# Optimization experiments

Hardware: AMD Instinct MI355X
Metric: run time of the kernel (lower is better)

The kernel has to match this reference:

```python
import jax, jax.numpy as jnp
import numpy as np

S, B, D = 2048, 2, 4096
H, KVH, HD = 32, 8, 128          # n_heads_q, n_kv_heads, head_dim
NREP = H // KVH                  # GQA repeat factor
ROPE_BASE = 10000.0


def _rope(x, cos, sin):
    # x: [B, S, h, HD]; cos/sin: [S, HD//2]
    xr = x.reshape(x.shape[:-1] + (-1, 2))
    x0, x1 = xr[..., 0], xr[..., 1]
    c = cos[None, :, None, :]
    s = sin[None, :, None, :]
    out = jnp.stack([x0 * c - x1 * s, x0 * s + x1 * c], axis=-1)
    return out.reshape(x.shape)


def setup_inputs() -> dict:
    key = jax.random.key(0)
    k0, k1, k2, k3, k4 = jax.random.split(key, 5)
    x = jax.random.normal(k0, (S, B, D), jnp.float32)
    inv_freq = 1.0 / (ROPE_BASE ** (np.arange(0, HD, 2, dtype=np.float64) / HD))  # [HD//2]
    t = np.arange(S, dtype=np.float64)[:, None] * inv_freq[None, :]               # [S, HD//2]
    freqs_cos = jnp.asarray(np.cos(t), jnp.float32)
    freqs_sin = jnp.asarray(np.sin(t), jnp.float32)
    scale = 0.02
    wq = jax.random.normal(k1, (H * HD, D), jnp.float32) * scale
    wk = jax.random.normal(k2, (KVH * HD, D), jnp.float32) * scale
    wv = jax.random.normal(k3, (KVH * HD, D), jnp.float32) * scale
    wo = jax.random.normal(k4, (D, H * HD), jnp.float32) * scale
    return {"x": x, "start_pos": 0, "freqs_cos": freqs_cos, "freqs_sin": freqs_sin,
            "wq": wq, "wk": wk, "wv": wv, "wo": wo}


def reference(x, start_pos, freqs_cos, freqs_sin, wq, wk, wv, wo):
    seq_len, batch, _ = x.shape
    # QKV projections (torch Linear: y = x @ W^T), then [S,B,*] -> [B,S,h,HD]
    q = (x @ wq.T).transpose(1, 0, 2).reshape(batch, seq_len, H, HD)
    k = (x @ wk.T).transpose(1, 0, 2).reshape(batch, seq_len, KVH, HD)
    v = (x @ wv.T).transpose(1, 0, 2).reshape(batch, seq_len, KVH, HD)
    # RoPE on q and k
    q = _rope(q, freqs_cos, freqs_sin)
    k = _rope(k, freqs_cos, freqs_sin)
    # repeat_kv (GQA)
    k = jnp.repeat(k, NREP, axis=2)
    v = jnp.repeat(v, NREP, axis=2)
    # [B, H, S, HD]
    q = q.transpose(0, 2, 1, 3)
    k = k.transpose(0, 2, 1, 3)
    v = v.transpose(0, 2, 1, 3)
    # causal scaled dot-product attention (SDPA is_causal=True equivalent)
    scores = jnp.einsum('bhqd,bhkd->bhqk', q, k) / np.float32(np.sqrt(HD))
    causal = jnp.tril(jnp.ones((seq_len, seq_len), dtype=bool))
    scores = jnp.where(causal[None, None], scores, jnp.float32(-jnp.inf))
    probs = jax.nn.softmax(scores.astype(jnp.float32), axis=-1).astype(q.dtype)
    out = jnp.einsum('bhqk,bhkd->bhqd', probs, v)
    # [B,H,S,HD] -> [B,S,H*HD] -> [S,B,H*HD]
    out = out.transpose(0, 2, 1, 3).reshape(batch, seq_len, H * HD).transpose(1, 0, 2)
    return out @ wo.T
```

## Files before the change

### kernel.cpp

```cpp
#include <hip/hip_runtime.h>

typedef __attribute__((ext_vector_type(8))) short s16x8;
typedef __attribute__((ext_vector_type(8))) __bf16 bf16x8;
typedef __attribute__((ext_vector_type(4))) float f32x4;

#define S_LEN 2048
#define KDIM  4096
#define CSOFT 0.12751743f

__device__ __forceinline__ unsigned short f2bf(float f) {
  unsigned u = __builtin_bit_cast(unsigned, f);
  u += 0x7fffu + ((u >> 16) & 1u);
  return (unsigned short)(u >> 16);
}

__device__ __forceinline__ f32x4 mfma_bf16(s16x8 a, s16x8 b, f32x4 c) {
  return __builtin_amdgcn_mfma_f32_16x16x32_bf16(
      __builtin_bit_cast(bf16x8, a), __builtin_bit_cast(bf16x8, b), c, 0, 0, 0);
}

__device__ __forceinline__ void gload_lds16(const unsigned short* g, void* l) {
  __builtin_amdgcn_global_load_lds(
      (const __attribute__((address_space(1))) void*)g,
      (__attribute__((address_space(3))) void*)l, 16, 0, 0);
}

__global__ void cvt_bf16(const float* __restrict__ in,
                         unsigned short* __restrict__ out, int n8) {
  int i = blockIdx.x * 256 + threadIdx.x;
  if (i >= n8) return;
  const float* p = in + (size_t)i * 8;
  f32x4 a = *(const f32x4*)(p);
  f32x4 b = *(const f32x4*)(p + 4);
  s16x8 v;
  v[0] = (short)f2bf(a[0]); v[1] = (short)f2bf(a[1]);
  v[2] = (short)f2bf(a[2]); v[3] = (short)f2bf(a[3]);
  v[4] = (short)f2bf(b[0]); v[5] = (short)f2bf(b[1]);
  v[6] = (short)f2bf(b[2]); v[7] = (short)f2bf(b[3]);
  *(s16x8*)(out + (size_t)i * 8) = v;
}

template <int EPI>
__global__ __launch_bounds__(512, 1)
void gemm256(const unsigned short* __restrict__ A,
             const unsigned short* __restrict__ B,
             void* __restrict__ Out,
             const float* __restrict__ cosT,
             const float* __restrict__ sinT) {
  const int K = KDIM;
  __shared__ __align__(16) unsigned short As[2 * 2 * 8192];
  __shared__ __align__(16) unsigned short Bs[2 * 2 * 8192];

  const int tid = threadIdx.x;
  const int lane = tid & 63, wid = tid >> 6;
  const int l15 = lane & 15, l4 = lane >> 4;
  const int wr = wid >> 2, wc = wid & 3;

  int bid = blockIdx.x;
  int wg = (bid & 7) * 32 + (bid >> 3);
  const int rt = wg >> 4, ct = wg & 15;
  const int row0 = rt * 256, col0 = ct * 256;

  const int ch0 = tid, ch1 = 512 + tid;
  const int sr0 = ch0 >> 3, u0 = (ch0 & 7) ^ (sr0 & 7);
  const int sr1 = ch1 >> 3, u1 = (ch1 & 7) ^ (sr1 & 7);
  const unsigned short* A0p = A + (size_t)(row0 + sr0) * K + u0 * 8;
  const unsigned short* A1p = A + (size_t)(row0 + sr1) * K + u1 * 8;
  const unsigned short* B0p = B + (size_t)(col0 + sr0) * K + u0 * 8;
  const unsigned short* B1p = B + (size_t)(col0 + sr1) * K + u1 * 8;

  const int rdo0 = l15 * 128 + ((l4 ^ (l15 & 7)) << 4);
  const int rdo1 = l15 * 128 + (((4 | l4) ^ (l15 & 7)) << 4);

  f32x4 acc[8][4];
#pragma unroll
  for (int m = 0; m < 8; m++)
#pragma unroll
    for (int n = 0; n < 4; n++) acc[m][n] = f32x4{0.f, 0.f, 0.f, 0.f};

  auto stageA = [&](int buf, int h, int kt) {
    char* d = (char*)As + buf * 32768 + h * 16384 + wid * 1024;
    size_t so = (size_t)h * 128 * K + kt;
    gload_lds16(A0p + so, d);
    gload_lds16(A1p + so, d + 8192);
  };
  auto stageB = [&](int buf, int h, int kt) {
    char* d = (char*)Bs + buf * 32768 + h * 16384 + wid * 1024;
    size_t so = (size_t)h * 128 * K + kt;
    gload_lds16(B0p + so, d);
    gload_lds16(B1p + so, d + 8192);
  };
  auto bar = [&]() {
    __builtin_amdgcn_s_barrier();
    __builtin_amdgcn_sched_barrier(0);
  };
  auto quad = [&](const s16x8* ak0, const s16x8* ak1,
                  const s16x8* bk0, const s16x8* bk1, int mb, int nb) {
    __builtin_amdgcn_s_setprio(1);
#pragma unroll
    for (int mi = 0; mi < 4; mi++)
#pragma unroll
      for (int ni = 0; ni < 2; ni++) {
        acc[mb + mi][nb + ni] =
            mfma_bf16(ak0[mi], bk0[ni], acc[mb + mi][nb + ni]);
        acc[mb + mi][nb + ni] =
            mfma_bf16(ak1[mi], bk1[ni], acc[mb + mi][nb + ni]);
      }
    __builtin_amdgcn_s_setprio(0);
  };

  auto tile4 = [&](int buf, auto st1, auto st2, auto st3, auto st4,
                   int vmEnd) {
    const char* Ab = (const char*)As + buf * 32768 + wr * 16384;
    const char* Bb = (const char*)Bs + buf * 32768 + (wc >> 1) * 16384 +
                     (wc & 1) * 8192;
    s16x8 a0k0[4], a0k1[4], a1k0[4], a1k1[4];
    s16x8 b0k0[2], b0k1[2], b1k0[2], b1k1[2];

#pragma unroll
    for (int mi = 0; mi < 4; mi++) {
      a0k0[mi] = *(const s16x8*)(Ab + mi * 2048 + rdo0);
      a0k1[mi] = *(const s16x8*)(Ab + mi * 2048 + rdo1);
    }
#pragma unroll
    for (int ni = 0; ni < 2; ni++) {
      b0k0[ni] = *(const s16x8*)(Bb + ni * 2048 + rdo0);
      b0k1[ni] = *(const s16x8*)(Bb + ni * 2048 + rdo1);
    }
    st1();
    bar();
    quad(a0k0, a0k1, b0k0, b0k1, 0, 0);
    bar();

#pragma unroll
    for (int mi = 0; mi < 4; mi++) {
      a1k0[mi] = *(const s16x8*)(Ab + 8192 + mi * 2048 + rdo0);
      a1k1[mi] = *(const s16x8*)(Ab + 8192 + mi * 2048 + rdo1);
    }
#pragma unroll
    for (int ni = 0; ni < 2; ni++) {
      b1k0[ni] = *(const s16x8*)(Bb + 4096 + ni * 2048 + rdo0);
      b1k1[ni] = *(const s16x8*)(Bb + 4096 + ni * 2048 + rdo1);
    }
    st2();
    bar();
    quad(a1k0, a1k1, b0k0, b0k1, 4, 0);
    bar();

    st3();
    bar();
    quad(a0k0, a0k1, b1k0, b1k1, 0, 2);
    bar();

    st4();
    bar();
    quad(a1k0, a1k1, b1k0, b1k1, 4, 2);
    if (vmEnd == 4) {
      asm volatile("s_waitcnt vmcnt(4)" ::: "memory");
    } else if (vmEnd == 0) {
      asm volatile("s_waitcnt vmcnt(0)" ::: "memory");
    }
    bar();
  };
  auto nop = [&]() {};

  stageA(0, 0, 0);
  stageA(0, 1, 0);
  stageB(0, 0, 0);
  stageB(0, 1, 0);
  stageA(1, 0, 64);
  stageA(1, 1, 64);
  asm volatile("s_waitcnt vmcnt(4)" ::: "memory");
  bar();

  for (int j = 0; j < 31; j++) {
    const int k1 = (2 * j + 1) * 64, k2 = (2 * j + 2) * 64,
              k3 = (2 * j + 3) * 64;
    tile4(0, [&] { stageB(1, 0, k1); }, [&] { stageB(1, 1, k1); },
          [&] { stageA(0, 0, k2); }, [&] { stageA(0, 1, k2); }, 4);
    tile4(1, [&] { stageB(0, 0, k2); }, [&] { stageB(0, 1, k2); },
          [&] { stageA(1, 0, k3); }, [&] { stageA(1, 1, k3); }, 4);
  }
  {
    const int k1 = 63 * 64;
    tile4(0, [&] { stageB(1, 0, k1); }, [&] { stageB(1, 1, k1); }, nop, nop,
          0);
    tile4(1, nop, nop, nop, nop, -1);
  }

#pragma unroll
  for (int m = 0; m < 8; m++) {
#pragma unroll
    for (int n = 0; n < 4; n++) {
      f32x4 v = acc[m][n];
      int rowb = row0 + wr * 128 + m * 16 + l4 * 4;
      int col = col0 + wc * 64 + n * 16 + l15;
      if (EPI == 3) {
        float* o = (float*)Out;
#pragma unroll
        for (int r = 0; r < 4; r++) o[(size_t)(rowb + r) * 4096 + col] = v[r];
      } else {
        float vp[4];
#pragma unroll
        for (int r = 0; r < 4; r++) vp[r] = __shfl_xor(v[r], 1, 64);
        bool odd = lane & 1;
        int fi = (col & 127) >> 1;
#pragma unroll
        for (int r = 0; r < 4; r++) {
          int nn = rowb + r, s = nn >> 1;
          float c = cosT[s * 64 + fi], sn = sinT[s * 64 + fi];
          v[r] = odd ? (vp[r] * sn + v[r] * c) : (v[r] * c - vp[r] * sn);
        }
        unsigned short* o = (unsigned short*)Out;
        int hh = col >> 7, hd = col & 127;
#pragma unroll
        for (int r = 0; r < 4; r++) {
          int nn = rowb + r, s = nn >> 1, b = nn & 1;
          o[((size_t)(b * 32 + hh) * 2048 + s) * 128 + hd] = f2bf(v[r]);
        }
      }
    }
  }
}

template <int EPI, int N, bool B_FP32>
__global__ __launch_bounds__(256, 2)
void gemm_bt(const unsigned short* __restrict__ A,
             const float* __restrict__ Bw32,
             const unsigned short* __restrict__ Bw16,
             void* __restrict__ Out,
             const float* __restrict__ cosT,
             const float* __restrict__ sinT) {
  const int K = KDIM;
  const int tid = threadIdx.x;
  const int lane = tid & 63, wid = tid >> 6;
  const int l15 = lane & 15, l4 = lane >> 4;
  const int nct = N / 128;
  const int ct = blockIdx.x % nct, rt = blockIdx.x / nct;
  const int row0 = rt * 128, col0 = ct * 128;
  const int wr = wid >> 1, wc = wid & 1;

  __shared__ __align__(16) unsigned short As[128 * 32];
  __shared__ __align__(16) unsigned short Bs[128 * 32];

  f32x4 acc[4][4];
#pragma unroll
  for (int i = 0; i < 4; i++)
#pragma unroll
    for (int j = 0; j < 4; j++) acc[i][j] = f32x4{0.f, 0.f, 0.f, 0.f};

  for (int kt = 0; kt < K; kt += 32) {
#pragma unroll
    for (int i = 0; i < 2; i++) {
      int j = wid * 2 + i;
      int ch = j * 64 + lane;
      int r = ch >> 2, c = ch & 3;
      int sc = c ^ ((r >> 1) & 3);
      gload_lds16(A + (size_t)(row0 + r) * K + kt + sc * 8, (char*)As + j * 1024);
    }
    if (B_FP32) {
#pragma unroll
      for (int j = 0; j < 2; j++) {
        int ch = tid + 256 * j;
        int r = ch >> 2, c = ch & 3;
        const float* src = Bw32 + (size_t)(col0 + r) * K + kt + c * 8;
        f32x4 f0 = *(const f32x4*)(src);
        f32x4 f1 = *(const f32x4*)(src + 4);
        s16x8 v;
        v[0] = (short)f2bf(f0[0]); v[1] = (short)f2bf(f0[1]);
        v[2] = (short)f2bf(f0[2]); v[3] = (short)f2bf(f0[3]);
        v[4] = (short)f2bf(f1[0]); v[5] = (short)f2bf(f1[1]);
        v[6] = (short)f2bf(f1[2]); v[7] = (short)f2bf(f1[3]);
        int sw = c ^ ((r >> 1) & 3);
        *(s16x8*)((char*)Bs + r * 64 + sw * 16) = v;
      }
    } else {
#pragma unroll
      for (int i = 0; i < 2; i++) {
        int j = wid * 2 + i;
        int ch = j * 64 + lane;
        int r = ch >> 2, c = ch & 3;
        int sc = c ^ ((r >> 1) & 3);
        gload_lds16(Bw16 + (size_t)(col0 + r) * K + kt + sc * 8, (char*)Bs + j * 1024);
      }
    }
    __syncthreads();

    s16x8 af[4], bfr[4];
#pragma unroll
    for (int mi = 0; mi < 4; mi++) {
      int r = wr * 64 + mi * 16 + l15;
      int sw = l4 ^ ((r >> 1) & 3);
      af[mi] = *(const s16x8*)((char*)As + r * 64 + sw * 16);
    }
#pragma unroll
    for (int ni = 0; ni < 4; ni++) {
      int r = wc * 64 + ni * 16 + l15;
      int sw = l4 ^ ((r >> 1) & 3);
      bfr[ni] = *(const s16x8*)((char*)Bs + r * 64 + sw * 16);
    }
#pragma unroll
    for (int mi = 0; mi < 4; mi++)
#pragma unroll
      for (int ni = 0; ni < 4; ni++)
        acc[mi][ni] = mfma_bf16(af[mi], bfr[ni], acc[mi][ni]);
    __syncthreads();
  }

#pragma unroll
  for (int mi = 0; mi < 4; mi++) {
#pragma unroll
    for (int ni = 0; ni < 4; ni++) {
      f32x4 v = acc[mi][ni];
      int rowb = row0 + wr * 64 + mi * 16 + l4 * 4;
      int col = col0 + wc * 64 + ni * 16 + l15;
      if (EPI == 3) {
        float* o = (float*)Out;
#pragma unroll
        for (int r = 0; r < 4; r++) o[(size_t)(rowb + r) * 4096 + col] = v[r];
      } else {
        if (EPI != 2) {
          float vp[4];
#pragma unroll
          for (int r = 0; r < 4; r++) vp[r] = __shfl_xor(v[r], 1, 64);
          bool odd = lane & 1;
          int fi = (col & 127) >> 1;
#pragma unroll
          for (int r = 0; r < 4; r++) {
            int n = rowb + r, s = n >> 1;
            float c = cosT[s * 64 + fi], sn = sinT[s * 64 + fi];
            v[r] = odd ? (vp[r] * sn + v[r] * c) : (v[r] * c - vp[r] * sn);
          }
        }
        unsigned short* o = (unsigned short*)Out;
        int hh = col >> 7, hd = col & 127;
#pragma unroll
        for (int r = 0; r < 4; r++) {
          int n = rowb + r, s = n >> 1, b = n & 1;
          size_t idx;
          if (EPI == 0)      idx = ((size_t)(b * 32 + hh) * 2048 + s) * 128 + hd;
          else if (EPI == 1) idx = ((size_t)(b * 8 + hh) * 2048 + s) * 128 + hd;
          else               idx = ((size_t)(b * 8 + hh) * 128 + hd) * 2048 + s;
          o[idx] = f2bf(v[r]);
        }
      }
    }
  }
}

__global__ __launch_bounds__(256, 2)
void attn_fwd(const unsigned short* __restrict__ Qa,
              const unsigned short* __restrict__ Ka,
              const unsigned short* __restrict__ Vt,
              unsigned short* __restrict__ AO) {
  int bid = blockIdx.x;
  int pid = bid & 7;
  int h = (bid >> 3) & 31;
  int b = bid >> 8;
  int kvh = h >> 2;
  int tid = threadIdx.x, lane = tid & 63, wid = tid >> 6;
  int l15 = lane & 15, l4 = lane >> 4;

  __shared__ __align__(16) unsigned short Ks[64 * 128];
  __shared__ __align__(16) unsigned short Vs[128 * 64];
  __shared__ __align__(16) unsigned short Ps[4][32 * 64];

  const unsigned short* Qp = Qa + ((size_t)(b * 32 + h) * 2048) * 128;
  const unsigned short* Kp = Ka + ((size_t)(b * 8 + kvh) * 2048) * 128;
  const unsigned short* Vp = Vt + ((size_t)(b * 8 + kvh) * 128) * 2048;

  for (int half = 0; half < 2; half++) {
    int qt = half == 0 ? (7 - pid) : (8 + pid);
    int q0 = qt * 128, qr0 = q0 + wid * 32;

    s16x8 qf[2][4];
#pragma unroll
    for (int mi = 0; mi < 2; mi++)
#pragma unroll
      for (int ks = 0; ks < 4; ks++)
        qf[mi][ks] = *(const s16x8*)(Qp + (size_t)(qr0 + mi * 16 + l15) * 128 +
                                     ks * 32 + l4 * 8);

    f32x4 o[2][8];
#pragma unroll
    for (int mi = 0; mi < 2; mi++)
#pragma unroll
      for (int nb = 0; nb < 8; nb++) o[mi][nb] = f32x4{0.f, 0.f, 0.f, 0.f};
    float m[2][4], lsum[2][4];
#pragma unroll
    for (int mi = 0; mi < 2; mi++)
#pragma unroll
      for (int pr = 0; pr < 4; pr++) { m[mi][pr] = -1e30f; lsum[mi][pr] = 0.f; }

    int nt = q0 / 64 + 2;
    for (int t = 0; t < nt; t++) {
      int s0 = t * 64;
      const unsigned short* ktp = Kp + (size_t)s0 * 128;
#pragma unroll
      for (int i = 0; i < 4; i++) {
        int j = wid * 4 + i;
        int ch = j * 64 + lane;
        {
          int r = ch >> 4, cl = ch & 15;
          int sc = (cl & 8) | ((cl ^ (r & 7)) & 7);
          gload_lds16(ktp + r * 128 + sc * 8, (char*)Ks + j * 1024);
        }
        {
          int r = ch >> 3, p = ch & 7;
          int sc = p ^ (r & 7);
          gload_lds16(Vp + (size_t)r * 2048 + s0 + sc * 8, (char*)Vs + j * 1024);
        }
      }
      __syncthreads();

      if (s0 <= qr0 + 31) {
        f32x4 sc[2][4];
#pragma unroll
        for (int mi = 0; mi < 2; mi++)
#pragma unroll
          for (int kb = 0; kb < 4; kb++) sc[mi][kb] = f32x4{0.f, 0.f, 0.f, 0.f};
#pragma unroll
        for (int kb = 0; kb < 4; kb++) {
          int r = kb * 16 + l15;
#pragma unroll
          for (int ks = 0; ks < 4; ks++) {
            int c = ks * 4 + l4;
            int sw = (c & 8) | ((c ^ (r & 7)) & 7);
            s16x8 kf = *(const s16x8*)((char*)Ks + r * 256 + sw * 16);
            sc[0][kb] = mfma_bf16(qf[0][ks], kf, sc[0][kb]);
            sc[1][kb] = mfma_bf16(qf[1][ks], kf, sc[1][kb]);
          }
        }
        bool needmask = (s0 + 63) > qr0;
#pragma unroll
        for (int mi = 0; mi < 2; mi++) {
          if (needmask) {
#pragma unroll
            for (int kb = 0; kb < 4; kb++) {
              int kg = s0 + kb * 16 + l15;
#pragma unroll
              for (int pr = 0; pr < 4; pr++) {
                int qg = qr0 + mi * 16 + l4 * 4 + pr;
                if (kg > qg) sc[mi][kb][pr] = -1e30f;
              }
            }
          }
          float rm[4];
#pragma unroll
          for (int pr = 0; pr < 4; pr++)
            rm[pr] = fmaxf(fmaxf(sc[mi][0][pr], sc[mi][1][pr]),
                           fmaxf(sc[mi][2][pr], sc[mi][3][pr]));
#pragma unroll
          for (int xm = 1; xm <= 8; xm <<= 1)
#pragma unroll
            for (int pr = 0; pr < 4; pr++)
              rm[pr] = fmaxf(rm[pr], __shfl_xor(rm[pr], xm, 64));
          bool grow = false;
#pragma unroll
          for (int pr = 0; pr < 4; pr++)
            grow = grow || ((rm[pr] - m[mi][pr]) * CSOFT > 8.f);
          if (__any(grow)) {
            float fac[4];
#pragma unroll
            for (int pr = 0; pr < 4; pr++) {
              float nm = fmaxf(m[mi][pr], rm[pr]);
              fac[pr] = __builtin_amdgcn_exp2f((m[mi][pr] - nm) * CSOFT);
              m[mi][pr] = nm;
              lsum[mi][pr] *= fac[pr];
            }
#pragma unroll
            for (int nb = 0; nb < 8; nb++)
#pragma unroll
              for (int pr = 0; pr < 4; pr++) o[mi][nb][pr] *= fac[pr];
          }
          float rs[4] = {0.f, 0.f, 0.f, 0.f};
#pragma unroll
          for (int kb = 0; kb < 4; kb++)
#pragma unroll
            for (int pr = 0; pr < 4; pr++) {
              float p = __builtin_amdgcn_exp2f((sc[mi][kb][pr] - m[mi][pr]) * CSOFT);
              sc[mi][kb][pr] = p;
              rs[pr] += p;
            }
#pragma unroll
          for (int xm = 1; xm <= 8; xm <<= 1)
#pragma unroll
            for (int pr = 0; pr < 4; pr++) rs[pr] += __shfl_xor(rs[pr], xm, 64);
#pragma unroll
          for (int pr = 0; pr < 4; pr++) lsum[mi][pr] += rs[pr];
          char* pb = (char*)(&Ps[wid][0]);
#pragma unroll
          for (int kb = 0; kb < 4; kb++) {
            int col = kb * 16 + l15;
#pragma unroll
            for (int pr = 0; pr < 4; pr++) {
              int row = mi * 16 + l4 * 4 + pr;
              *(unsigned short*)(pb + row * 128 + (((col >> 3) ^ (row & 7)) * 16) +
                                 (col & 7) * 2) = f2bf(sc[mi][kb][pr]);
            }
          }
        }
        char* pb = (char*)(&Ps[wid][0]);
#pragma unroll
        for (int ks = 0; ks < 2; ks++) {
          s16x8 pa[2];
#pragma unroll
          for (int mi = 0; mi < 2; mi++) {
            int row = mi * 16 + l15;
            int c = ks * 4 + l4;
            pa[mi] = *(const s16x8*)(pb + row * 128 + ((c ^ (row & 7)) * 16));
          }
#pragma unroll
          for (int nb = 0; nb < 8; nb++) {
            int r = nb * 16 + l15;
            int c = ks * 4 + l4;
            s16x8 vf = *(const s16x8*)((char*)Vs + r * 128 + ((c ^ (r & 7)) * 16));
            o[0][nb] = mfma_bf16(pa[0], vf, o[0][nb]);
            o[1][nb] = mfma_bf16(pa[1], vf, o[1][nb]);
          }
        }
      }
      __syncthreads();
    }

#pragma unroll
    for (int mi = 0; mi < 2; mi++) {
      float inv[4];
#pragma unroll
      for (int pr = 0; pr < 4; pr++) inv[pr] = 1.f / lsum[mi][pr];
#pragma unroll
      for (int nb = 0; nb < 8; nb++) {
        int col = h * 128 + nb * 16 + l15;
#pragma unroll
        for (int pr = 0; pr < 4; pr++) {
          int q = qr0 + mi * 16 + l4 * 4 + pr;
          AO[(size_t)(q * 2 + b) * 4096 + col] = f2bf(o[mi][nb][pr] * inv[pr]);
        }
      }
    }
  }
}

extern "C" void kernel_launch(void* const* d_in, const int* in_sizes, int n_in,
                              void* d_out, int out_size, void* d_ws, size_t ws_size,
                              hipStream_t stream) {
  const float* x = (const float*)d_in[0];
  const float* cosT = (const float*)d_in[2];
  const float* sinT = (const float*)d_in[3];
  const float* wq = (const float*)d_in[4];
  const float* wk = (const float*)d_in[5];
  const float* wv = (const float*)d_in[6];
  const float* wo = (const float*)d_in[7];
  float* out = (float*)d_out;

  char* ws = (char*)d_ws;
  unsigned short* xb = (unsigned short*)(ws);
  unsigned short* Qa = (unsigned short*)(ws + 33554432ull);
  unsigned short* Ka = (unsigned short*)(ws + 67108864ull);
  unsigned short* Vt = (unsigned short*)(ws + 75497472ull);
  unsigned short* AO = (unsigned short*)(ws + 83886080ull);
  unsigned short* wqb = (unsigned short*)(ws + 117440512ull);
  unsigned short* wkb = (unsigned short*)(ws + 150994944ull);
  unsigned short* wvb = (unsigned short*)(ws + 159383552ull);
  unsigned short* wob = (unsigned short*)(ws + 167772160ull);
  bool wcvt = ws_size >= 201326592ull;

  cvt_bf16<<<8192, 256, 0, stream>>>(x, xb, 2097152);
  if (wcvt) {
    cvt_bf16<<<8192, 256, 0, stream>>>(wq, wqb, 2097152);
    cvt_bf16<<<2048, 256, 0, stream>>>(wk, wkb, 524288);
    cvt_bf16<<<2048, 256, 0, stream>>>(wv, wvb, 524288);
    cvt_bf16<<<8192, 256, 0, stream>>>(wo, wob, 2097152);
    gemm256<0><<<256, 512, 0, stream>>>(xb, wqb, Qa, cosT, sinT);
    gemm_bt<1, 1024, false><<<256, 256, 0, stream>>>(xb, nullptr, wkb, Ka, cosT, sinT);
    gemm_bt<2, 1024, false><<<256, 256, 0, stream>>>(xb, nullptr, wvb, Vt, cosT, sinT);
  } else {
    gemm_bt<0, 4096, true><<<1024, 256, 0, stream>>>(xb, wq, nullptr, Qa, cosT, sinT);
    gemm_bt<1, 1024, true><<<256, 256, 0, stream>>>(xb, wk, nullptr, Ka, cosT, sinT);
    gemm_bt<2, 1024, true><<<256, 256, 0, stream>>>(xb, wv, nullptr, Vt, cosT, sinT);
  }
  attn_fwd<<<512, 256, 0, stream>>>(Qa, Ka, Vt, AO);
  if (wcvt) {
    gemm256<3><<<256, 512, 0, stream>>>(AO, wob, out, cosT, sinT);
  } else {
    gemm_bt<3, 4096, true><<<1024, 256, 0, stream>>>(AO, wo, nullptr, out, cosT, sinT);
  }
}
```

Baseline: 626.4 us.

## Fuse bf16 conversions into one launch, remap blocks per XCD, add MFMA priority

Merges the five fp32→bf16 conversion launches into a single cvt_all kernel, which removes launch gaps. It also remaps gemm256 and attention block indices so each XCD works on a contiguous tile region or KV-head group, aiming for better L2 reuse. It adds s_setprio around the attention MFMA loops and drops the sched_barrier from the gemm barrier. The index remapping changes which blocks share an L2, and removing the sched_barrier lets the compiler reorder work across barriers.

Measured after the change: 619.4 us. Within noise of the previous version (-1.1%).

```diff
diff --git a/kernel.cpp b/kernel.cpp
--- a/kernel.cpp
+++ b/kernel.cpp
@@ -25,11 +25,7 @@
       (__attribute__((address_space(3))) void*)l, 16, 0, 0);
 }
 
-__global__ void cvt_bf16(const float* __restrict__ in,
-                         unsigned short* __restrict__ out, int n8) {
-  int i = blockIdx.x * 256 + threadIdx.x;
-  if (i >= n8) return;
-  const float* p = in + (size_t)i * 8;
+__device__ __forceinline__ void cvt8(const float* p, unsigned short* out) {
   f32x4 a = *(const f32x4*)(p);
   f32x4 b = *(const f32x4*)(p + 4);
   s16x8 v;
@@ -37,7 +33,33 @@
   v[2] = (short)f2bf(a[2]); v[3] = (short)f2bf(a[3]);
   v[4] = (short)f2bf(b[0]); v[5] = (short)f2bf(b[1]);
   v[6] = (short)f2bf(b[2]); v[7] = (short)f2bf(b[3]);
-  *(s16x8*)(out + (size_t)i * 8) = v;
+  *(s16x8*)(out) = v;
+}
+
+__global__ void cvt_bf16(const float* __restrict__ in,
+                         unsigned short* __restrict__ out, int n8) {
+  int i = blockIdx.x * 256 + threadIdx.x;
+  if (i >= n8) return;
+  cvt8(in + (size_t)i * 8, out + (size_t)i * 8);
+}
+
+__global__ void cvt_all(const float* __restrict__ x, const float* __restrict__ wq,
+                        const float* __restrict__ wk, const float* __restrict__ wv,
+                        const float* __restrict__ wo,
+                        unsigned short* __restrict__ ox, unsigned short* __restrict__ oq,
+                        unsigned short* __restrict__ ok, unsigned short* __restrict__ ov,
+                        unsigned short* __restrict__ oo) {
+  int blk = blockIdx.x;
+  const float* src;
+  unsigned short* dst;
+  int i;
+  if (blk < 8192) { src = x; dst = ox; i = blk; }
+  else if (blk < 16384) { src = wq; dst = oq; i = blk - 8192; }
+  else if (blk < 18432) { src = wk; dst = ok; i = blk - 16384; }
+  else if (blk < 20480) { src = wv; dst = ov; i = blk - 18432; }
+  else { src = wo; dst = oo; i = blk - 20480; }
+  size_t idx = ((size_t)i * 256 + threadIdx.x) * 8;
+  cvt8(src + idx, dst + idx);
 }
 
 template <int EPI>
@@ -57,8 +79,11 @@
   const int wr = wid >> 2, wc = wid & 3;
 
   int bid = blockIdx.x;
-  int wg = (bid & 7) * 32 + (bid >> 3);
-  const int rt = wg >> 4, ct = wg & 15;
+  {
+  }
+  const int xcd = bid & 7, ii = bid >> 3;
+  const int rt = (xcd >> 1) * 4 + (ii >> 3);
+  const int ct = (xcd & 1) * 8 + (ii & 7);
   const int row0 = rt * 256, col0 = ct * 256;
 
   const int ch0 = tid, ch1 = 512 + tid;
@@ -90,10 +115,7 @@
     gload_lds16(B0p + so, d);
     gload_lds16(B1p + so, d + 8192);
   };
-  auto bar = [&]() {
-    __builtin_amdgcn_s_barrier();
-    __builtin_amdgcn_sched_barrier(0);
-  };
+  auto bar = [&]() { __builtin_amdgcn_s_barrier(); };
   auto quad = [&](const s16x8* ak0, const s16x8* ak1,
                   const s16x8* bk0, const s16x8* bk1, int mb, int nb) {
     __builtin_amdgcn_s_setprio(1);
@@ -354,10 +376,12 @@
               const unsigned short* __restrict__ Vt,
               unsigned short* __restrict__ AO) {
   int bid = blockIdx.x;
-  int pid = bid & 7;
-  int h = (bid >> 3) & 31;
-  int b = bid >> 8;
-  int kvh = h >> 2;
+  int xcd = bid & 7, slot = bid >> 3;
+  int grp = xcd + 8 * (slot >> 5);
+  int idx = slot & 31;
+  int b = grp >> 3, kvh = grp & 7;
+  int pid = idx & 7;
+  int h = kvh * 4 + ((idx >> 3) & 3);
   int tid = threadIdx.x, lane = tid & 63, wid = tid >> 6;
   int l15 = lane & 15, l4 = lane >> 4;
 
@@ -419,6 +443,7 @@
         for (int mi = 0; mi < 2; mi++)
 #pragma unroll
           for (int kb = 0; kb < 4; kb++) sc[mi][kb] = f32x4{0.f, 0.f, 0.f, 0.f};
+        __builtin_amdgcn_s_setprio(1);
 #pragma unroll
         for (int kb = 0; kb < 4; kb++) {
           int r = kb * 16 + l15;
@@ -431,6 +456,7 @@
             sc[1][kb] = mfma_bf16(qf[1][ks], kf, sc[1][kb]);
           }
         }
+        __builtin_amdgcn_s_setprio(0);
         bool needmask = (s0 + 63) > qr0;
 #pragma unroll
         for (int mi = 0; mi < 2; mi++) {
@@ -501,6 +527,7 @@
           }
         }
         char* pb = (char*)(&Ps[wid][0]);
+        __builtin_amdgcn_s_setprio(1);
 #pragma unroll
         for (int ks = 0; ks < 2; ks++) {
           s16x8 pa[2];
@@ -519,6 +546,7 @@
             o[1][nb] = mfma_bf16(pa[1], vf, o[1][nb]);
           }
         }
+        __builtin_amdgcn_s_setprio(0);
       }
       __syncthreads();
     }
@@ -565,16 +593,13 @@
   unsigned short* wob = (unsigned short*)(ws + 167772160ull);
   bool wcvt = ws_size >= 201326592ull;
 
-  cvt_bf16<<<8192, 256, 0, stream>>>(x, xb, 2097152);
   if (wcvt) {
-    cvt_bf16<<<8192, 256, 0, stream>>>(wq, wqb, 2097152);
-    cvt_bf16<<<2048, 256, 0, stream>>>(wk, wkb, 524288);
-    cvt_bf16<<<2048, 256, 0, stream>>>(wv, wvb, 524288);
-    cvt_bf16<<<8192, 256, 0, stream>>>(wo, wob, 2097152);
+    cvt_all<<<28672, 256, 0, stream>>>(x, wq, wk, wv, wo, xb, wqb, wkb, wvb, wob);
     gemm256<0><<<256, 512, 0, stream>>>(xb, wqb, Qa, cosT, sinT);
     gemm_bt<1, 1024, false><<<256, 256, 0, stream>>>(xb, nullptr, wkb, Ka, cosT, sinT);
     gemm_bt<2, 1024, false><<<256, 256, 0, stream>>>(xb, nullptr, wvb, Vt, cosT, sinT);
   } else {
+    cvt_bf16<<<8192, 256, 0, stream>>>(x, xb, 2097152);
     gemm_bt<0, 4096, true><<<1024, 256, 0, stream>>>(xb, wq, nullptr, Qa, cosT, sinT);
     gemm_bt<1, 1024, true><<<256, 256, 0, stream>>>(xb, wk, nullptr, Ka, cosT, sinT);
     gemm_bt<2, 1024, true><<<256, 256, 0, stream>>>(xb, wv, nullptr, Vt, cosT, sinT);
```
